# Kernel optimization log

Hardware: AMD Instinct MI355X
Metric: run time of the kernel (lower is better)

The kernel has to match this reference:

```python
import jax, jax.numpy as jnp
import numpy as np

B, T, D, H = 4096, 16, 512, 8
DH = D // H
EPS = 1e-5

def _layer_norm(x, w, b):
    mu = jnp.mean(x, axis=-1, keepdims=True)
    var = jnp.mean(jnp.square(x - mu), axis=-1, keepdims=True)
    return (x - mu) * jax.lax.rsqrt(var + EPS) * w + b

def setup_inputs() -> dict:
    key = jax.random.key(0)
    ks = jax.random.split(key, 12)
    inp = {
        'structural_output': jax.random.normal(ks[0], (B, T, D), jnp.float32),
        'position_embedding_clustering_coefficient': jax.random.normal(ks[1], (B, T, D), jnp.float32),
        'position_embedding_bidirectional_links_ratio': jax.random.normal(ks[2], (B, T, D), jnp.float32),
        'exist_nodes': jax.random.randint(ks[3], (B, T), 0, 2, jnp.int32),
        'pos_emb': jax.random.normal(ks[4], (T, D), jnp.float32) * 0.02,
        'Qw': jax.random.normal(ks[5], (D, D), jnp.float32) / np.sqrt(D),
        'Kw': jax.random.normal(ks[6], (D, D), jnp.float32) / np.sqrt(D),
        'Vw': jax.random.normal(ks[7], (D, D), jnp.float32) / np.sqrt(D),
        'ln_w': jnp.ones((D,), jnp.float32),
        'ln_b': jnp.zeros((D,), jnp.float32),
        'ff1_w': jax.random.normal(ks[8], (D, D), jnp.float32) / np.sqrt(D),
        'ff1_b': jnp.zeros((D,), jnp.float32),
        'prelu_a': jnp.array(0.25, jnp.float32),
        'ff2_w': jax.random.normal(ks[9], (2, D), jnp.float32) / np.sqrt(D),
        'ff2_b': jnp.zeros((2,), jnp.float32),
    }
    return inp

def reference(structural_output, position_embedding_clustering_coefficient,
              position_embedding_bidirectional_links_ratio, exist_nodes,
              pos_emb, Qw, Kw, Vw, ln_w, ln_b, ff1_w, ff1_b, prelu_a, ff2_w, ff2_b):
    x = structural_output
    # temporal input = x + positional embeddings, then shared LayerNorm
    t_in = _layer_norm(
        x + pos_emb[None, :, :]
        + position_embedding_clustering_coefficient
        + position_embedding_bidirectional_links_ratio,
        ln_w, ln_b)
    # fused-style QKV projections, split into heads [B,T,H,DH]
    q = (t_in @ Qw).reshape(B, T, H, DH)
    k = (t_in @ Kw).reshape(B, T, H, DH)
    v = (t_in @ Vw).reshape(B, T, H, DH)
    scores = jnp.einsum('bihd,bjhd->bhij', q, k) / np.sqrt(DH)  # [B,H,T,T]
    causal = jnp.tril(jnp.ones((T, T), bool))
    scores = jnp.where(causal[None, None], scores, jnp.float32(-1e9))
    attn = jax.nn.softmax(scores, axis=-1)  # dropout is identity at inference
    out = jnp.einsum('bhij,bjhd->bihd', attn, v).reshape(B, T, D)
    # residual with pre-norm input, shared LayerNorm again
    y = _layer_norm(out + x, ln_w, ln_b)
    # feed forward: Linear(D,D) -> PReLU -> Linear(D,2)
    h = y @ ff1_w.T + ff1_b
    h = jnp.maximum(h, 0) + prelu_a * jnp.minimum(h, 0)
    return h @ ff2_w.T + ff2_b
```

## Files before the change

### kernel.cpp

```cpp
#include <hip/hip_runtime.h>

#define NROWS 65536
#define DD 512
#define EPS_LN 1e-5f

typedef __bf16 bfx8 __attribute__((ext_vector_type(8)));
typedef float fx4 __attribute__((ext_vector_type(4)));

__device__ __forceinline__ unsigned short f2bf(float f) {
  unsigned int u = __builtin_bit_cast(unsigned int, f);
  u += 0x7fffu + ((u >> 16) & 1u);
  return (unsigned short)(u >> 16);
}
__device__ __forceinline__ float bflo(unsigned int u) { return __builtin_bit_cast(float, u << 16); }
__device__ __forceinline__ float bfhi(unsigned int u) { return __builtin_bit_cast(float, u & 0xffff0000u); }
__device__ __forceinline__ unsigned int pack2(float a, float b) {
  return (unsigned int)f2bf(a) | ((unsigned int)f2bf(b) << 16);
}
__device__ __forceinline__ float wave_sum(float v) {
  #pragma unroll
  for (int off = 32; off; off >>= 1) v += __shfl_xor(v, off);
  return v;
}
__device__ __forceinline__ void glds16(const unsigned short* g, unsigned short* l) {
  __builtin_amdgcn_global_load_lds(
      (const __attribute__((address_space(1))) unsigned int*)g,
      (__attribute__((address_space(3))) unsigned int*)l, 16, 0, 0);
}

__global__ __launch_bounds__(256) void prep_weights(
    const float* __restrict__ Qw, const float* __restrict__ Kw, const float* __restrict__ Vw,
    const float* __restrict__ ff1w, const float* __restrict__ b2,
    unsigned short* __restrict__ WqkvT, unsigned short* __restrict__ W1T,
    float* __restrict__ out) {
  int idx = blockIdx.x * 256 + threadIdx.x;
  if (idx < 1536 * 512) {
    int j = idx >> 9, k = idx & 511;
    const float* src = (j < 512) ? Qw : (j < 1024 ? Kw : Vw);
    WqkvT[idx] = f2bf(src[k * 512 + (j & 511)]);
  } else if (idx < 1536 * 512 + 512 * 512) {
    int i2 = idx - 1536 * 512;
    W1T[i2] = f2bf(ff1w[i2]);
  } else {
    int i3 = idx - (1536 * 512 + 512 * 512);
    if (i3 < NROWS * 2) out[i3] = b2[i3 & 1];
  }
}

__global__ __launch_bounds__(256) void ln1_kernel(
    const float* __restrict__ x, const float* __restrict__ pcc, const float* __restrict__ pblr,
    const float* __restrict__ pos, const float* __restrict__ lnw, const float* __restrict__ lnb,
    unsigned short* __restrict__ t_in) {
  int row = blockIdx.x * 4 + (threadIdx.x >> 6);
  int lane = threadIdx.x & 63;
  size_t base = (size_t)row * DD + lane * 8;
  int t = row & 15;
  const fx4* x4 = (const fx4*)(x + base);
  const fx4* p4 = (const fx4*)(pcc + base);
  const fx4* q4 = (const fx4*)(pblr + base);
  const fx4* e4 = (const fx4*)(pos + t * DD + lane * 8);
  fx4 a0 = x4[0], a1 = x4[1], b0 = p4[0], b1 = p4[1], c0 = q4[0], c1 = q4[1], d0 = e4[0], d1 = e4[1];
  float s[8];
  #pragma unroll
  for (int j = 0; j < 4; ++j) { s[j] = a0[j] + b0[j] + c0[j] + d0[j]; s[j+4] = a1[j] + b1[j] + c1[j] + d1[j]; }
  float sum = 0.f;
  #pragma unroll
  for (int j = 0; j < 8; ++j) sum += s[j];
  sum = wave_sum(sum);
  float mu = sum * (1.0f / 512.0f);
  float vs = 0.f;
  #pragma unroll
  for (int j = 0; j < 8; ++j) { float d = s[j] - mu; vs += d * d; }
  vs = wave_sum(vs);
  float rs = rsqrtf(vs * (1.0f / 512.0f) + EPS_LN);
  const fx4* w4 = (const fx4*)(lnw + lane * 8);
  const fx4* bb4 = (const fx4*)(lnb + lane * 8);
  fx4 w0 = w4[0], w1 = w4[1], g0 = bb4[0], g1 = bb4[1];
  float o[8];
  #pragma unroll
  for (int j = 0; j < 4; ++j) { o[j] = (s[j] - mu) * rs * w0[j] + g0[j]; o[j+4] = (s[j+4] - mu) * rs * w1[j] + g1[j]; }
  uint4 pk;
  pk.x = pack2(o[0], o[1]); pk.y = pack2(o[2], o[3]); pk.z = pack2(o[4], o[5]); pk.w = pack2(o[6], o[7]);
  *(uint4*)(t_in + base) = pk;
}

template<bool FUSE>
__global__ __launch_bounds__(256) void gemm_bt(
    const unsigned short* __restrict__ A, const unsigned short* __restrict__ BT,
    unsigned short* __restrict__ C, int ldc,
    const float* __restrict__ bias, const float* __restrict__ prelu_a,
    const float* __restrict__ w2, float* __restrict__ out) {
  __shared__ unsigned short As[128 * 64];
  __shared__ unsigned short Bs[128 * 64];
  int tid = threadIdx.x;
  int col0 = blockIdx.x * 128, row0 = blockIdx.y * 128;
  int wid = tid >> 6, lane = tid & 63;
  int wm = (wid >> 1) * 64, wn = (wid & 1) * 64;
  int srow = (lane >> 3);
  int skk = (lane & 7) * 8;
  fx4 acc[4][4] = {};
  for (int k0 = 0; k0 < 512; k0 += 64) {
    #pragma unroll
    for (int c = 0; c < 4; ++c) {
      int chunk = wid * 4 + c;
      int r = chunk * 8 + srow;
      glds16(A + (size_t)(row0 + r) * 512 + k0 + skk, As + chunk * 512);
      glds16(BT + (size_t)(col0 + r) * 512 + k0 + skk, Bs + chunk * 512);
    }
    __syncthreads();
    #pragma unroll
    for (int ks = 0; ks < 2; ++ks) {
      int koff = ks * 32 + (lane >> 4) * 8;
      bfx8 af[4], bfr[4];
      #pragma unroll
      for (int m = 0; m < 4; ++m) af[m] = *(const bfx8*)(As + (wm + m * 16 + (lane & 15)) * 64 + koff);
      #pragma unroll
      for (int n = 0; n < 4; ++n) bfr[n] = *(const bfx8*)(Bs + (wn + n * 16 + (lane & 15)) * 64 + koff);
      #pragma unroll
      for (int m = 0; m < 4; ++m)
        #pragma unroll
        for (int n = 0; n < 4; ++n)
          acc[m][n] = __builtin_amdgcn_mfma_f32_16x16x32_bf16(af[m], bfr[n], acc[m][n], 0, 0, 0);
    }
    __syncthreads();
  }
  int fq = lane >> 4, fr = lane & 15;
  if constexpr (!FUSE) {
    #pragma unroll
    for (int m = 0; m < 4; ++m) {
      #pragma unroll
      for (int n = 0; n < 4; ++n) {
        int rbase = row0 + wm + m * 16 + fq * 4;
        int cidx = col0 + wn + n * 16 + fr;
        #pragma unroll
        for (int r = 0; r < 4; ++r)
          C[(size_t)(rbase + r) * ldc + cidx] = f2bf(acc[m][n][r]);
      }
    }
  } else {
    float pa = *prelu_a;
    float p0[16] = {}, p1[16] = {};
    #pragma unroll
    for (int n = 0; n < 4; ++n) {
      int cidx = col0 + wn + n * 16 + fr;
      float bv = bias[cidx];
      float wa = w2[cidx], wb = w2[512 + cidx];
      #pragma unroll
      for (int m = 0; m < 4; ++m) {
        #pragma unroll
        for (int r = 0; r < 4; ++r) {
          float v = acc[m][n][r] + bv;
          v = fmaxf(v, 0.f) + pa * fminf(v, 0.f);
          p0[m * 4 + r] += v * wa;
          p1[m * 4 + r] += v * wb;
        }
      }
    }
    #pragma unroll
    for (int off = 1; off < 16; off <<= 1) {
      #pragma unroll
      for (int t = 0; t < 16; ++t) {
        p0[t] += __shfl_xor(p0[t], off);
        p1[t] += __shfl_xor(p1[t], off);
      }
    }
    if (fr == 0) {
      #pragma unroll
      for (int m = 0; m < 4; ++m) {
        #pragma unroll
        for (int r = 0; r < 4; ++r) {
          int row = row0 + wm + m * 16 + fq * 4 + r;
          __hip_atomic_fetch_add(&out[(size_t)row * 2 + 0], p0[m * 4 + r],
                                 __ATOMIC_RELAXED, __HIP_MEMORY_SCOPE_AGENT);
          __hip_atomic_fetch_add(&out[(size_t)row * 2 + 1], p1[m * 4 + r],
                                 __ATOMIC_RELAXED, __HIP_MEMORY_SCOPE_AGENT);
        }
      }
    }
  }
}

__global__ __launch_bounds__(256) void attn_ln2_kernel(
    const unsigned short* __restrict__ qkv, const float* __restrict__ x,
    const float* __restrict__ lnw, const float* __restrict__ lnb,
    unsigned short* __restrict__ y) {
  __shared__ unsigned short q_s[16 * 520];
  __shared__ unsigned short k_s[16 * 520];
  __shared__ unsigned short v_s[16 * 520];
  __shared__ float p_s[8 * 16 * 18];
  int b = blockIdx.x, tid = threadIdx.x;
  #pragma unroll
  for (int c = 0; c < 12; ++c) {
    int v = c * 256 + tid;
    int i = v / 192, colv = v % 192, col = colv * 8;
    uint4 d = *(const uint4*)(qkv + (size_t)(b * 16 + i) * 1536 + col);
    unsigned short* dst = (col < 512) ? (q_s + i * 520 + col)
                        : (col < 1024) ? (k_s + i * 520 + (col - 512))
                                       : (v_s + i * 520 + (col - 1024));
    *(uint4*)dst = d;
  }
  __syncthreads();
  if (tid < 128) {
    int h = tid >> 4, i = tid & 15;
    uint4 qv[8];
    #pragma unroll
    for (int db = 0; db < 8; ++db) qv[db] = *(const uint4*)(q_s + i * 520 + h * 64 + db * 8);
    float sc[16];
    float mx = -3e38f;
    #pragma unroll
    for (int j = 0; j < 16; ++j) {
      float acc = 0.f;
      const unsigned short* kr = k_s + j * 520 + h * 64;
      #pragma unroll
      for (int db = 0; db < 8; ++db) {
        uint4 kv = *(const uint4*)(kr + db * 8);
        acc += bflo(qv[db].x) * bflo(kv.x) + bfhi(qv[db].x) * bfhi(kv.x);
        acc += bflo(qv[db].y) * bflo(kv.y) + bfhi(qv[db].y) * bfhi(kv.y);
        acc += bflo(qv[db].z) * bflo(kv.z) + bfhi(qv[db].z) * bfhi(kv.z);
        acc += bflo(qv[db].w) * bflo(kv.w) + bfhi(qv[db].w) * bfhi(kv.w);
      }
      acc = (j <= i) ? acc * 0.125f : -3e38f;
      sc[j] = acc;
      mx = fmaxf(mx, acc);
    }
    float sum = 0.f;
    #pragma unroll
    for (int j = 0; j < 16; ++j) {
      float e = (j <= i) ? __expf(sc[j] - mx) : 0.f;
      sc[j] = e; sum += e;
    }
    float inv = 1.0f / sum;
    float* prow = p_s + (h * 16 + i) * 18;
    #pragma unroll
    for (int j = 0; j < 16; ++j) prow[j] = sc[j] * inv;
  }
  __syncthreads();
  int lane = tid & 63;
  #pragma unroll
  for (int rep = 0; rep < 4; ++rep) {
    int i = rep * 4 + (tid >> 6);
    int col = lane * 8, h = col >> 6;
    const float* prow = p_s + (h * 16 + i) * 18;
    float o[8] = {0, 0, 0, 0, 0, 0, 0, 0};
    #pragma unroll
    for (int j = 0; j < 16; ++j) {
      float p = prow[j];
      uint4 vv = *(const uint4*)(v_s + j * 520 + col);
      o[0] += p * bflo(vv.x); o[1] += p * bfhi(vv.x);
      o[2] += p * bflo(vv.y); o[3] += p * bfhi(vv.y);
      o[4] += p * bflo(vv.z); o[5] += p * bfhi(vv.z);
      o[6] += p * bflo(vv.w); o[7] += p * bfhi(vv.w);
    }
    size_t base = (size_t)(b * 16 + i) * 512 + col;
    const fx4* x4 = (const fx4*)(x + base);
    fx4 xa = x4[0], xb = x4[1];
    float s[8];
    #pragma unroll
    for (int j = 0; j < 4; ++j) { s[j] = o[j] + xa[j]; s[j+4] = o[j+4] + xb[j]; }
    float sum = 0.f;
    #pragma unroll
    for (int j = 0; j < 8; ++j) sum += s[j];
    sum = wave_sum(sum);
    float mu = sum * (1.0f / 512.0f);
    float vs = 0.f;
    #pragma unroll
    for (int j = 0; j < 8; ++j) { float d = s[j] - mu; vs += d * d; }
    vs = wave_sum(vs);
    float rs = rsqrtf(vs * (1.0f / 512.0f) + EPS_LN);
    const fx4* w4 = (const fx4*)(lnw + col);
    const fx4* bb4 = (const fx4*)(lnb + col);
    fx4 w0 = w4[0], w1 = w4[1], g0 = bb4[0], g1 = bb4[1];
    float oo[8];
    #pragma unroll
    for (int j = 0; j < 4; ++j) { oo[j] = (s[j] - mu) * rs * w0[j] + g0[j]; oo[j+4] = (s[j+4] - mu) * rs * w1[j] + g1[j]; }
    uint4 pk;
    pk.x = pack2(oo[0], oo[1]); pk.y = pack2(oo[2], oo[3]); pk.z = pack2(oo[4], oo[5]); pk.w = pack2(oo[6], oo[7]);
    *(uint4*)(y + base) = pk;
  }
}

extern "C" void kernel_launch(void* const* d_in, const int* in_sizes, int n_in,
                              void* d_out, int out_size, void* d_ws, size_t ws_size,
                              hipStream_t stream) {
  const float* x    = (const float*)d_in[0];
  const float* pcc  = (const float*)d_in[1];
  const float* pblr = (const float*)d_in[2];
  const float* pos  = (const float*)d_in[4];
  const float* Qw   = (const float*)d_in[5];
  const float* Kw   = (const float*)d_in[6];
  const float* Vw   = (const float*)d_in[7];
  const float* lnw  = (const float*)d_in[8];
  const float* lnb  = (const float*)d_in[9];
  const float* ff1w = (const float*)d_in[10];
  const float* ff1b = (const float*)d_in[11];
  const float* pra  = (const float*)d_in[12];
  const float* ff2w = (const float*)d_in[13];
  const float* ff2b = (const float*)d_in[14];
  float* out = (float*)d_out;

  char* ws = (char*)d_ws;
  unsigned short* WqkvT = (unsigned short*)ws;
  unsigned short* W1T   = (unsigned short*)(ws + 1572864);
  unsigned short* t_in  = (unsigned short*)(ws + 2097152);
  unsigned short* qkv   = (unsigned short*)(ws + 2097152 + 67108864);
  unsigned short* ybuf  = qkv;

  prep_weights<<<4608, 256, 0, stream>>>(Qw, Kw, Vw, ff1w, ff2b, WqkvT, W1T, out);
  ln1_kernel<<<NROWS / 4, 256, 0, stream>>>(x, pcc, pblr, pos, lnw, lnb, t_in);
  gemm_bt<false><<<dim3(1536 / 128, NROWS / 128), 256, 0, stream>>>(
      t_in, WqkvT, qkv, 1536, nullptr, nullptr, nullptr, nullptr);
  attn_ln2_kernel<<<4096, 256, 0, stream>>>(qkv, x, lnw, lnb, ybuf);
  gemm_bt<true><<<dim3(512 / 128, NROWS / 128), 256, 0, stream>>>(
      ybuf, W1T, nullptr, 0, ff1b, pra, ff2w, out);
}
```

Baseline: 808.0 us.

## Swizzle GEMM LDS layout, remap workgroups per XCD, split FF2 into separate kernel

The GEMM's shared-memory tiles now use an XOR swizzle on the 16-byte k-chunks, applied to both the global-to-LDS writes and the fragment reads, to cut bank conflicts. A 1D grid with XCD-aware block remapping replaces the 2D grid, aiming for better L2 locality. The fused FF1+PReLU+FF2 epilogue, which used shuffle reductions and atomics, is replaced by writing bf16 PReLU output to a buffer and running a separate row-wise FF2 reduction kernel. This removes the atomics and the output pre-initialisation, at the cost of an extra 64 MB write and read plus an additional kernel launch.

```diff
diff --git a/kernel.cpp b/kernel.cpp
--- a/kernel.cpp
+++ b/kernel.cpp
@@ -30,20 +30,16 @@
 
 __global__ __launch_bounds__(256) void prep_weights(
     const float* __restrict__ Qw, const float* __restrict__ Kw, const float* __restrict__ Vw,
-    const float* __restrict__ ff1w, const float* __restrict__ b2,
-    unsigned short* __restrict__ WqkvT, unsigned short* __restrict__ W1T,
-    float* __restrict__ out) {
+    const float* __restrict__ ff1w,
+    unsigned short* __restrict__ WqkvT, unsigned short* __restrict__ W1T) {
   int idx = blockIdx.x * 256 + threadIdx.x;
   if (idx < 1536 * 512) {
     int j = idx >> 9, k = idx & 511;
     const float* src = (j < 512) ? Qw : (j < 1024 ? Kw : Vw);
     WqkvT[idx] = f2bf(src[k * 512 + (j & 511)]);
-  } else if (idx < 1536 * 512 + 512 * 512) {
+  } else {
     int i2 = idx - 1536 * 512;
     W1T[i2] = f2bf(ff1w[i2]);
-  } else {
-    int i3 = idx - (1536 * 512 + 512 * 512);
-    if (i3 < NROWS * 2) out[i3] = b2[i3 & 1];
   }
 }
 
@@ -84,20 +80,23 @@
   *(uint4*)(t_in + base) = pk;
 }
 
-template<bool FUSE>
+template<int NT, bool EPI>
 __global__ __launch_bounds__(256) void gemm_bt(
     const unsigned short* __restrict__ A, const unsigned short* __restrict__ BT,
     unsigned short* __restrict__ C, int ldc,
-    const float* __restrict__ bias, const float* __restrict__ prelu_a,
-    const float* __restrict__ w2, float* __restrict__ out) {
+    const float* __restrict__ bias, const float* __restrict__ prelu_a) {
   __shared__ unsigned short As[128 * 64];
   __shared__ unsigned short Bs[128 * 64];
   int tid = threadIdx.x;
-  int col0 = blockIdx.x * 128, row0 = blockIdx.y * 128;
+  int nwg = gridDim.x;
+  int bid = blockIdx.x;
+  int cpx = nwg >> 3;
+  int swz = (bid & 7) * cpx + (bid >> 3);
+  int col0 = (swz % NT) * 128, row0 = (swz / NT) * 128;
   int wid = tid >> 6, lane = tid & 63;
   int wm = (wid >> 1) * 64, wn = (wid & 1) * 64;
   int srow = (lane >> 3);
-  int skk = (lane & 7) * 8;
+  int skk = (((lane & 7) ^ srow) & 7) * 8;
   fx4 acc[4][4] = {};
   for (int k0 = 0; k0 < 512; k0 += 64) {
     #pragma unroll
@@ -110,12 +109,12 @@
     __syncthreads();
     #pragma unroll
     for (int ks = 0; ks < 2; ++ks) {
-      int koff = ks * 32 + (lane >> 4) * 8;
+      int soff = ((ks * 4 + (lane >> 4)) ^ (lane & 7)) * 8;
       bfx8 af[4], bfr[4];
       #pragma unroll
-      for (int m = 0; m < 4; ++m) af[m] = *(const bfx8*)(As + (wm + m * 16 + (lane & 15)) * 64 + koff);
-      #pragma unroll
-      for (int n = 0; n < 4; ++n) bfr[n] = *(const bfx8*)(Bs + (wn + n * 16 + (lane & 15)) * 64 + koff);
+      for (int m = 0; m < 4; ++m) af[m] = *(const bfx8*)(As + (wm + m * 16 + (lane & 15)) * 64 + soff);
+      #pragma unroll
+      for (int n = 0; n < 4; ++n) bfr[n] = *(const bfx8*)(Bs + (wn + n * 16 + (lane & 15)) * 64 + soff);
       #pragma unroll
       for (int m = 0; m < 4; ++m)
         #pragma unroll
@@ -125,56 +124,19 @@
     __syncthreads();
   }
   int fq = lane >> 4, fr = lane & 15;
-  if constexpr (!FUSE) {
-    #pragma unroll
-    for (int m = 0; m < 4; ++m) {
-      #pragma unroll
-      for (int n = 0; n < 4; ++n) {
-        int rbase = row0 + wm + m * 16 + fq * 4;
-        int cidx = col0 + wn + n * 16 + fr;
-        #pragma unroll
-        for (int r = 0; r < 4; ++r)
-          C[(size_t)(rbase + r) * ldc + cidx] = f2bf(acc[m][n][r]);
-      }
-    }
-  } else {
-    float pa = *prelu_a;
-    float p0[16] = {}, p1[16] = {};
+  float pa = EPI ? *prelu_a : 0.f;
+  #pragma unroll
+  for (int m = 0; m < 4; ++m) {
     #pragma unroll
     for (int n = 0; n < 4; ++n) {
+      int rbase = row0 + wm + m * 16 + fq * 4;
       int cidx = col0 + wn + n * 16 + fr;
-      float bv = bias[cidx];
-      float wa = w2[cidx], wb = w2[512 + cidx];
-      #pragma unroll
-      for (int m = 0; m < 4; ++m) {
-        #pragma unroll
-        for (int r = 0; r < 4; ++r) {
-          float v = acc[m][n][r] + bv;
-          v = fmaxf(v, 0.f) + pa * fminf(v, 0.f);
-          p0[m * 4 + r] += v * wa;
-          p1[m * 4 + r] += v * wb;
-        }
-      }
-    }
-    #pragma unroll
-    for (int off = 1; off < 16; off <<= 1) {
-      #pragma unroll
-      for (int t = 0; t < 16; ++t) {
-        p0[t] += __shfl_xor(p0[t], off);
-        p1[t] += __shfl_xor(p1[t], off);
-      }
-    }
-    if (fr == 0) {
-      #pragma unroll
-      for (int m = 0; m < 4; ++m) {
-        #pragma unroll
-        for (int r = 0; r < 4; ++r) {
-          int row = row0 + wm + m * 16 + fq * 4 + r;
-          __hip_atomic_fetch_add(&out[(size_t)row * 2 + 0], p0[m * 4 + r],
-                                 __ATOMIC_RELAXED, __HIP_MEMORY_SCOPE_AGENT);
-          __hip_atomic_fetch_add(&out[(size_t)row * 2 + 1], p1[m * 4 + r],
-                                 __ATOMIC_RELAXED, __HIP_MEMORY_SCOPE_AGENT);
-        }
+      float bv = EPI ? bias[cidx] : 0.f;
+      #pragma unroll
+      for (int r = 0; r < 4; ++r) {
+        float v = acc[m][n][r];
+        if constexpr (EPI) { v += bv; v = fmaxf(v, 0.f) + pa * fminf(v, 0.f); }
+        C[(size_t)(rbase + r) * ldc + cidx] = f2bf(v);
       }
     }
   }
@@ -276,6 +238,33 @@
     uint4 pk;
     pk.x = pack2(oo[0], oo[1]); pk.y = pack2(oo[2], oo[3]); pk.z = pack2(oo[4], oo[5]); pk.w = pack2(oo[6], oo[7]);
     *(uint4*)(y + base) = pk;
+  }
+}
+
+__global__ __launch_bounds__(256) void ff2_kernel(
+    const unsigned short* __restrict__ h, const float* __restrict__ w2,
+    const float* __restrict__ b2, float* __restrict__ out) {
+  int row = blockIdx.x * 4 + (threadIdx.x >> 6);
+  int lane = threadIdx.x & 63;
+  size_t base = (size_t)row * DD + lane * 8;
+  uint4 hv = *(const uint4*)(h + base);
+  float f[8];
+  f[0] = bflo(hv.x); f[1] = bfhi(hv.x); f[2] = bflo(hv.y); f[3] = bfhi(hv.y);
+  f[4] = bflo(hv.z); f[5] = bfhi(hv.z); f[6] = bflo(hv.w); f[7] = bfhi(hv.w);
+  const fx4* w0p = (const fx4*)(w2 + lane * 8);
+  const fx4* w1p = (const fx4*)(w2 + 512 + lane * 8);
+  fx4 w00 = w0p[0], w01 = w0p[1], w10 = w1p[0], w11 = w1p[1];
+  float a0 = 0.f, a1 = 0.f;
+  #pragma unroll
+  for (int j = 0; j < 4; ++j) {
+    a0 += f[j] * w00[j] + f[j+4] * w01[j];
+    a1 += f[j] * w10[j] + f[j+4] * w11[j];
+  }
+  a0 = wave_sum(a0);
+  a1 = wave_sum(a1);
+  if (lane == 0) {
+    out[(size_t)row * 2 + 0] = a0 + b2[0];
+    out[(size_t)row * 2 + 1] = a1 + b2[1];
   }
 }
 
@@ -304,12 +293,14 @@
   unsigned short* t_in  = (unsigned short*)(ws + 2097152);
   unsigned short* qkv   = (unsigned short*)(ws + 2097152 + 67108864);
   unsigned short* ybuf  = qkv;
-
-  prep_weights<<<4608, 256, 0, stream>>>(Qw, Kw, Vw, ff1w, ff2b, WqkvT, W1T, out);
+  unsigned short* hbuf  = t_in;
+
+  prep_weights<<<4096, 256, 0, stream>>>(Qw, Kw, Vw, ff1w, WqkvT, W1T);
   ln1_kernel<<<NROWS / 4, 256, 0, stream>>>(x, pcc, pblr, pos, lnw, lnb, t_in);
-  gemm_bt<false><<<dim3(1536 / 128, NROWS / 128), 256, 0, stream>>>(
-      t_in, WqkvT, qkv, 1536, nullptr, nullptr, nullptr, nullptr);
+  gemm_bt<12, false><<<12 * (NROWS / 128), 256, 0, stream>>>(
+      t_in, WqkvT, qkv, 1536, nullptr, nullptr);
   attn_ln2_kernel<<<4096, 256, 0, stream>>>(qkv, x, lnw, lnb, ybuf);
-  gemm_bt<true><<<dim3(512 / 128, NROWS / 128), 256, 0, stream>>>(
-      ybuf, W1T, nullptr, 0, ff1b, pra, ff2w, out);
-}
+  gemm_bt<4, true><<<4 * (NROWS / 128), 256, 0, stream>>>(
+      ybuf, W1T, hbuf, 512, ff1b, pra);
+  ff2_kernel<<<NROWS / 4, 256, 0, stream>>>(hbuf, ff2w, ff2b, out);
+}
```

Measured after the change: 753.8 us. 6.7% less time.
